# Optimization experiments

Measured on AMD Instinct MI355X. Metric: run time of the kernel, lower is better.

Reference implementation:

```python
import jax, jax.numpy as jnp
import numpy as np

N = 50000   # nodes
E = 600000  # edges
R = 8       # relations
B = 8       # bases
D = 128     # feature dim (in = hidden = out)
H = 4       # GAT heads
NEG = 0.1   # leaky_relu slope between layers
LN_EPS = 1e-5


def layer_norm(x, g, b):
    mu = jnp.mean(x, axis=-1, keepdims=True)
    var = jnp.mean(jnp.square(x - mu), axis=-1, keepdims=True)
    return (x - mu) * jax.lax.rsqrt(var + LN_EPS) * g + b


def rgcn(x, basis, comp, root, bias, src, dst, etype):
    # W[r] = sum_b comp[r,b] * basis[b]  -> [R, D, D]
    W = jnp.einsum('rb,bio->rio', comp, basis)
    h = jnp.einsum('ni,rio->rno', x, W)          # [R, N, D] per-relation transform
    msg = h[etype, src]                          # [E, D] gather per edge
    seg = etype.astype(jnp.int32) * N + dst      # (relation, dst) segment id
    deg = jax.ops.segment_sum(jnp.ones((src.shape[0],), x.dtype), seg, num_segments=R * N)
    inv = 1.0 / jnp.maximum(deg, 1.0)            # mean aggregation per relation
    out = jax.ops.segment_sum(msg * inv[seg][:, None], dst, num_segments=N)
    return out + x @ root + bias


def gat(x, W, a_src, a_dst, bias, src, dst):
    h = (x @ W).reshape(N, H, D)                 # [N, H, D]
    loop = jnp.arange(N, dtype=src.dtype)        # add self loops
    s2 = jnp.concatenate([src, loop])
    d2 = jnp.concatenate([dst, loop])
    hs = h[s2]                                   # [E+N, H, D]
    e = jnp.sum(hs * a_src, -1) + jnp.sum(h[d2] * a_dst, -1)   # [E+N, H]
    e = jax.nn.leaky_relu(e, 0.2)
    m = jax.ops.segment_max(e, d2, num_segments=N)              # stable softmax per dst
    ex = jnp.exp(e - m[d2])
    denom = jax.ops.segment_sum(ex, d2, num_segments=N)
    coef = ex / denom[d2]                        # [E+N, H]
    out = jax.ops.segment_sum(coef[..., None] * hs, d2, num_segments=N)  # [N, H, D]
    return jnp.mean(out, axis=1) + bias          # concat=False -> head mean


def setup_inputs():
    key = jax.random.key(0)
    ks = jax.random.split(key, 20)
    nrm = lambda k, shp, s=0.1: jax.random.normal(k, shp, dtype=jnp.float32) * s
    inp = {
        'x': jax.random.normal(ks[0], (N, D), dtype=jnp.float32),
        'edge_index': jax.random.randint(ks[1], (2, E), 0, N, dtype=jnp.int32),
        'edge_type': jax.random.randint(ks[2], (E,), 0, R, dtype=jnp.int32),
        'r0_basis': nrm(ks[3], (B, D, D)), 'r0_comp': nrm(ks[4], (R, B)),
        'r0_root': nrm(ks[5], (D, D)), 'r0_bias': jnp.zeros((D,), jnp.float32),
        'ln0_g': jnp.ones((D,), jnp.float32), 'ln0_b': jnp.zeros((D,), jnp.float32),
        'r1_basis': nrm(ks[6], (B, D, D)), 'r1_comp': nrm(ks[7], (R, B)),
        'r1_root': nrm(ks[8], (D, D)), 'r1_bias': jnp.zeros((D,), jnp.float32),
        'ln1_g': jnp.ones((D,), jnp.float32), 'ln1_b': jnp.zeros((D,), jnp.float32),
        'gat_w': nrm(ks[9], (D, H * D)), 'gat_asrc': nrm(ks[10], (H, D)),
        'gat_adst': nrm(ks[11], (H, D)), 'gat_bias': jnp.zeros((D,), jnp.float32),
        'ln2_g': jnp.ones((D,), jnp.float32), 'ln2_b': jnp.zeros((D,), jnp.float32),
        'r2_basis': nrm(ks[12], (B, D, D)), 'r2_comp': nrm(ks[13], (R, B)),
        'r2_root': nrm(ks[14], (D, D)), 'r2_bias': jnp.zeros((D,), jnp.float32),
    }
    return inp


def reference(x, edge_index, edge_type,
              r0_basis, r0_comp, r0_root, r0_bias, ln0_g, ln0_b,
              r1_basis, r1_comp, r1_root, r1_bias, ln1_g, ln1_b,
              gat_w, gat_asrc, gat_adst, gat_bias, ln2_g, ln2_b,
              r2_basis, r2_comp, r2_root, r2_bias):
    src, dst = edge_index[0], edge_index[1]
    h = rgcn(x, r0_basis, r0_comp, r0_root, r0_bias, src, dst, edge_type)
    h = jax.nn.leaky_relu(layer_norm(h, ln0_g, ln0_b), NEG)
    h = rgcn(h, r1_basis, r1_comp, r1_root, r1_bias, src, dst, edge_type)
    h = jax.nn.leaky_relu(layer_norm(h, ln1_g, ln1_b), NEG)
    h = gat(h, gat_w, gat_asrc, gat_adst, gat_bias, src, dst)
    h = jax.nn.leaky_relu(layer_norm(h, ln2_g, ln2_b), NEG)
    h = rgcn(h, r2_basis, r2_comp, r2_root, r2_bias, src, dst, edge_type)
    # F.normalize(p=2, dim=1)
    return h / jnp.maximum(jnp.linalg.norm(h, axis=1, keepdims=True), 1e-12)
```

## Files before the change

kernel.cpp:

```cpp
#include <hip/hip_runtime.h>
#include <hip/hip_bf16.h>

#define DD 128
#define NKEY8 8
#define LDA_AGG 1056
#define SRCM 0x00FFFFFF

using bf16x8 = __attribute__((ext_vector_type(8))) __bf16;
using f32x4  = __attribute__((ext_vector_type(4))) float;

__device__ __forceinline__ float leaky(float x, float s){ return x > 0.f ? x : s * x; }
__device__ __forceinline__ float bflo(unsigned u){ return __uint_as_float(u << 16); }
__device__ __forceinline__ float bfhi(unsigned u){ return __uint_as_float(u & 0xffff0000u); }
__device__ __forceinline__ unsigned bfpack(float x, float y){
  __hip_bfloat16 hx = __float2bfloat16(x), hy = __float2bfloat16(y);
  unsigned short ux = *reinterpret_cast<unsigned short*>(&hx);
  unsigned short uy = *reinterpret_cast<unsigned short*>(&hy);
  return (unsigned)ux | ((unsigned)uy << 16);
}

__global__ void k_hist(const int* __restrict__ dst, const int* __restrict__ et,
                       int* __restrict__ cnt, int E_){
  int e = blockIdx.x * 256 + threadIdx.x;
  if (e < E_) atomicAdd(&cnt[dst[e] * NKEY8 + et[e]], 1);
}

__global__ void k_scan1(const int* __restrict__ cnt, int* __restrict__ ptr,
                        int* __restrict__ part, int n){
  __shared__ int sm[256];
  int tid = threadIdx.x;
  int base = blockIdx.x * 1024 + tid * 4;
  int a0 = base + 0 < n ? cnt[base + 0] : 0;
  int a1 = base + 1 < n ? cnt[base + 1] : 0;
  int a2 = base + 2 < n ? cnt[base + 2] : 0;
  int a3 = base + 3 < n ? cnt[base + 3] : 0;
  int s = a0 + a1 + a2 + a3;
  sm[tid] = s; __syncthreads();
  for (int off = 1; off < 256; off <<= 1){
    int v = tid >= off ? sm[tid - off] : 0;
    __syncthreads(); sm[tid] += v; __syncthreads();
  }
  int ex = sm[tid] - s;
  if (tid == 255) part[blockIdx.x] = sm[255];
  if (base + 0 < n) ptr[base + 0] = ex;
  if (base + 1 < n) ptr[base + 1] = ex + a0;
  if (base + 2 < n) ptr[base + 2] = ex + a0 + a1;
  if (base + 3 < n) ptr[base + 3] = ex + a0 + a1 + a2;
}

__global__ void k_scan2(int* __restrict__ part, int nb){
  __shared__ int sm[512];
  int tid = threadIdx.x;
  int v = tid < nb ? part[tid] : 0;
  sm[tid] = v; __syncthreads();
  for (int off = 1; off < 512; off <<= 1){
    int u = tid >= off ? sm[tid - off] : 0;
    __syncthreads(); sm[tid] += u; __syncthreads();
  }
  if (tid < nb) part[tid] = sm[tid] - v;
}

__global__ void k_scan3(int* __restrict__ ptr, const int* __restrict__ part, int n, int E_){
  int i = blockIdx.x * 256 + threadIdx.x;
  if (i < n) ptr[i] += part[i >> 10];
  if (i == n) ptr[n] = E_;
}

__global__ void k_inv(const int* __restrict__ ptr, float* __restrict__ inv, int n){
  int i = blockIdx.x * 256 + threadIdx.x;
  if (i < n) inv[i] = 1.0f / fmaxf((float)(ptr[i + 1] - ptr[i]), 1.0f);
}

__global__ void k_scatter_pos(const int* __restrict__ src, const int* __restrict__ dst,
                              const int* __restrict__ et, int* __restrict__ run,
                              int* __restrict__ epk, int E_){
  int e = blockIdx.x * 256 + threadIdx.x;
  if (e >= E_) return;
  int r = et[e];
  int pos = atomicAdd(&run[dst[e] * NKEY8 + r], 1);
  epk[pos] = (r << 24) | src[e];
}

__global__ void k_cvt(const float* __restrict__ in, __hip_bfloat16* __restrict__ out, int n){
  int i = blockIdx.x * 256 + threadIdx.x;
  if (i < n) out[i] = __float2bfloat16(in[i]);
}

__global__ void k_makeW(const float* __restrict__ basis, const float* __restrict__ comp,
                        const float* __restrict__ root, __hip_bfloat16* __restrict__ Wp){
  int idx = blockIdx.x * 256 + threadIdx.x;
  int k = idx >> 7, n = idx & 127;
  float v;
  if (k < 1024){
    int r = k >> 7, i = k & 127;
    float s = 0.f;
    #pragma unroll
    for (int b = 0; b < 8; b++) s += comp[r * 8 + b] * basis[b * 16384 + i * 128 + n];
    v = s;
  } else {
    v = root[(k - 1024) * 128 + n];
  }
  int kt = k >> 5, kr = k & 31;
  int lane = (n & 15) | ((kr >> 3) << 4);
  int ii = kr & 7, nt = n >> 4;
  Wp[((size_t)(kt * 8 + nt) * 64 + lane) * 8 + ii] = __float2bfloat16(v);
}

__global__ void k_packGZ(const float* __restrict__ Wg, __hip_bfloat16* __restrict__ Wp){
  int idx = blockIdx.x * 256 + threadIdx.x;
  int k = idx >> 7, n = idx & 127;
  int h = k >> 7, i = k & 127;
  float v = Wg[(size_t)i * 512 + h * 128 + n];
  int kt = k >> 5, kr = k & 31;
  int lane = (n & 15) | ((kr >> 3) << 4);
  int ii = kr & 7, nt = n >> 4;
  Wp[((size_t)(kt * 8 + nt) * 64 + lane) * 8 + ii] = __float2bfloat16(v);
}

__global__ void k_valpha(const float* __restrict__ Wg, const float* __restrict__ a_src,
                         const float* __restrict__ a_dst, float* __restrict__ vT){
  int id = blockIdx.x * 256 + threadIdx.x;
  int sd = id >> 9, h = (id >> 7) & 3, i = id & 127;
  const float* a = (sd ? a_dst : a_src) + h * 128;
  const float* w = Wg + (size_t)i * 512 + h * 128;
  float s = 0.f;
  #pragma unroll 4
  for (int o = 0; o < 128; o++) s += w[o] * a[o];
  vT[(size_t)sd * 512 + h * 128 + i] = s;
}

__global__ void k_av(const __hip_bfloat16* __restrict__ xb, const float* __restrict__ vT,
                     float* __restrict__ aS, float* __restrict__ aD, int N_){
  int node = blockIdx.x * 4 + (threadIdx.x >> 6);
  if (node >= N_) return;
  int lane = threadIdx.x & 63;
  int h = lane >> 4, dg = lane & 15;
  uint4 u = *(const uint4*)(xb + (size_t)node * DD + dg * 8);
  const float* vs = vT + h * 128 + dg * 8;
  const float* vd = vT + 512 + h * 128 + dg * 8;
  float ss = 0.f, sd = 0.f;
  #pragma unroll
  for (int w = 0; w < 4; w++){
    unsigned uw = ((const unsigned*)&u)[w];
    float f0 = bflo(uw), f1 = bfhi(uw);
    ss += f0 * vs[w * 2] + f1 * vs[w * 2 + 1];
    sd += f0 * vd[w * 2] + f1 * vd[w * 2 + 1];
  }
  for (int o = 1; o < 16; o <<= 1){ ss += __shfl_xor(ss, o); sd += __shfl_xor(sd, o); }
  if (dg == 0){ aS[(size_t)node * 4 + h] = ss; aD[(size_t)node * 4 + h] = sd; }
}

__global__ void k_csr_agg(const int* __restrict__ ptr, const int* __restrict__ epk,
                          const float* __restrict__ inv, const __hip_bfloat16* __restrict__ xb,
                          __hip_bfloat16* __restrict__ agg, int N_){
  int w = threadIdx.x >> 6, lane = threadIdx.x & 63;
  int t = blockIdx.x * 4 + w;
  if (t >= N_) return;
  int beg = ptr[t * 8], end = ptr[t * 8 + 8];
  const __hip_bfloat16* xcol = xb + lane * 2;
  __hip_bfloat16* aggrow = agg + (size_t)t * LDA_AGG + lane * 2;
  const float* invrow = inv + (size_t)t * 8;
  float a0 = 0.f, a1 = 0.f;
  int cur = -1;
  unsigned written = 0;

#define CSR_FLUSH() { float iv = invrow[cur]; \
    *(unsigned*)(aggrow + cur * 128) = bfpack(a0 * iv, a1 * iv); \
    written |= (1u << cur); }
#define CSR_PROC(PK, U) { int r_ = (PK) >> 24; \
    if (r_ != cur){ if (cur >= 0){ CSR_FLUSH(); } cur = r_; a0 = 0.f; a1 = 0.f; } \
    a0 += bflo(U); a1 += bfhi(U); }

  int e = beg;
  for (; e + 4 <= end; e += 4){
    int pk0 = epk[e], pk1 = epk[e + 1], pk2 = epk[e + 2], pk3 = epk[e + 3];
    unsigned u0 = *(const unsigned*)(xcol + (size_t)(pk0 & SRCM) * DD);
    unsigned u1 = *(const unsigned*)(xcol + (size_t)(pk1 & SRCM) * DD);
    unsigned u2 = *(const unsigned*)(xcol + (size_t)(pk2 & SRCM) * DD);
    unsigned u3 = *(const unsigned*)(xcol + (size_t)(pk3 & SRCM) * DD);
    CSR_PROC(pk0, u0); CSR_PROC(pk1, u1); CSR_PROC(pk2, u2); CSR_PROC(pk3, u3);
  }
  for (; e < end; e++){
    int pk0 = epk[e];
    unsigned u0 = *(const unsigned*)(xcol + (size_t)(pk0 & SRCM) * DD);
    CSR_PROC(pk0, u0);
  }
  if (cur >= 0){ CSR_FLUSH(); }
  #pragma unroll
  for (int r = 0; r < 8; r++)
    if (!(written & (1u << r))) *(unsigned*)(aggrow + r * 128) = 0u;
#undef CSR_PROC
#undef CSR_FLUSH
}

__global__ void k_zagg(const int* __restrict__ ptr, const int* __restrict__ epk,
                       const float* __restrict__ cf, const float* __restrict__ cfS,
                       const float* __restrict__ den, const __hip_bfloat16* __restrict__ xb,
                       __hip_bfloat16* __restrict__ z, int N_){
  int w = threadIdx.x >> 6, lane = threadIdx.x & 63;
  int t = blockIdx.x * 4 + w;
  if (t >= N_) return;
  int dg = lane & 31, ep = lane >> 5;
  int beg = ptr[t * 8], end = ptr[t * 8 + 8];
  float acc[4][4];
  #pragma unroll
  for (int h = 0; h < 4; h++)
    #pragma unroll
    for (int j = 0; j < 4; j++) acc[h][j] = 0.f;
  const __hip_bfloat16* xbase = xb + dg * 4;
  for (int e = beg + ep; e < end; e += 2){
    int s = epk[e] & SRCM;
    uint2 v = *(const uint2*)(xbase + (size_t)s * DD);
    float4 c = *(const float4*)(cf + (size_t)e * 4);
    float f0 = bflo(v.x), f1 = bfhi(v.x), f2 = bflo(v.y), f3 = bfhi(v.y);
    const float* cp = (const float*)&c;
    #pragma unroll
    for (int h = 0; h < 4; h++){
      acc[h][0] += cp[h] * f0; acc[h][1] += cp[h] * f1;
      acc[h][2] += cp[h] * f2; acc[h][3] += cp[h] * f3;
    }
  }
  #pragma unroll
  for (int h = 0; h < 4; h++)
    #pragma unroll
    for (int j = 0; j < 4; j++) acc[h][j] += __shfl_xor(acc[h][j], 32);
  if (ep == 0){
    uint2 v = *(const uint2*)(xbase + (size_t)t * DD);
    float f0 = bflo(v.x), f1 = bfhi(v.x), f2 = bflo(v.y), f3 = bfhi(v.y);
    float4 cs = *(const float4*)(cfS + (size_t)t * 4);
    float4 dn = *(const float4*)(den + (size_t)t * 4);
    const float* csp = (const float*)&cs;
    const float* dnp = (const float*)&dn;
    #pragma unroll
    for (int h = 0; h < 4; h++){
      float sc = 0.25f / dnp[h];
      float y0 = (acc[h][0] + csp[h] * f0) * sc;
      float y1 = (acc[h][1] + csp[h] * f1) * sc;
      float y2 = (acc[h][2] + csp[h] * f2) * sc;
      float y3 = (acc[h][3] + csp[h] * f3) * sc;
      uint2 o; o.x = bfpack(y0, y1); o.y = bfpack(y2, y3);
      *(uint2*)(z + (size_t)t * 512 + h * 128 + dg * 4) = o;
    }
  }
}

template<int MODE>
__launch_bounds__(256)
__global__ void k_gemm_mfma(const __hip_bfloat16* __restrict__ A1, int lda1, int K1,
                            const __hip_bfloat16* __restrict__ A2, int K2,
                            int M, const __hip_bfloat16* __restrict__ Bp, int ntt,
                            const float* __restrict__ bias,
                            const float* __restrict__ ln_g, const float* __restrict__ ln_b,
                            float* __restrict__ Cf, __hip_bfloat16* __restrict__ Cb,
                            int ldc){
  int wave = threadIdx.x >> 6, lane = threadIdx.x & 63;
  int nt0 = blockIdx.y << 3;
  int mbase = blockIdx.x * 128 + wave * 32;
  int r0 = min(mbase + (lane & 15), M - 1);
  int r1 = min(mbase + 16 + (lane & 15), M - 1);
  int koff = (lane >> 4) << 3;
  f32x4 acc[2][8];
  #pragma unroll
  for (int i = 0; i < 2; i++)
    #pragma unroll
    for (int j = 0; j < 8; j++) acc[i][j] = (f32x4){0.f, 0.f, 0.f, 0.f};

  int ktile = 0;
  {
    const __hip_bfloat16* a0p = A1 + (size_t)r0 * lda1 + koff;
    const __hip_bfloat16* a1p = A1 + (size_t)r1 * lda1 + koff;
    for (int k0 = 0; k0 < K1; k0 += 32, ++ktile){
      bf16x8 a0 = *(const bf16x8*)(a0p + k0);
      bf16x8 a1 = *(const bf16x8*)(a1p + k0);
      const bf16x8* bfr = (const bf16x8*)(Bp + (((size_t)ktile * ntt + nt0) * 64 + lane) * 8);
      #pragma unroll
      for (int nt = 0; nt < 8; nt++){
        bf16x8 b = bfr[(size_t)nt * 64];
        acc[0][nt] = __builtin_amdgcn_mfma_f32_16x16x32_bf16(a0, b, acc[0][nt], 0, 0, 0);
        acc[1][nt] = __builtin_amdgcn_mfma_f32_16x16x32_bf16(a1, b, acc[1][nt], 0, 0, 0);
      }
    }
  }
  if (A2){
    const __hip_bfloat16* a0p = A2 + (size_t)r0 * DD + koff;
    const __hip_bfloat16* a1p = A2 + (size_t)r1 * DD + koff;
    for (int k0 = 0; k0 < K2; k0 += 32, ++ktile){
      bf16x8 a0 = *(const bf16x8*)(a0p + k0);
      bf16x8 a1 = *(const bf16x8*)(a1p + k0);
      const bf16x8* bfr = (const bf16x8*)(Bp + (((size_t)ktile * ntt + nt0) * 64 + lane) * 8);
      #pragma unroll
      for (int nt = 0; nt < 8; nt++){
        bf16x8 b = bfr[(size_t)nt * 64];
        acc[0][nt] = __builtin_amdgcn_mfma_f32_16x16x32_bf16(a0, b, acc[0][nt], 0, 0, 0);
        acc[1][nt] = __builtin_amdgcn_mfma_f32_16x16x32_bf16(a1, b, acc[1][nt], 0, 0, 0);
      }
    }
  }

  const int colb = lane & 15;
  const int lq = lane >> 4;

  float bias8[8], g8[8], b8[8];
  #pragma unroll
  for (int nt = 0; nt < 8; nt++){
    int c = (nt << 4) + colb;
    bias8[nt] = bias ? bias[c] : 0.f;
    if (MODE == 1){ g8[nt] = ln_g[c]; b8[nt] = ln_b[c]; }
  }

  #pragma unroll
  for (int mt = 0; mt < 2; mt++){
    #pragma unroll
    for (int j = 0; j < 4; j++){
      int row = mbase + mt * 16 + lq * 4 + j;
      if (MODE == 1){
        float v[8]; float s = 0.f;
        #pragma unroll
        for (int nt = 0; nt < 8; nt++){ v[nt] = acc[mt][nt][j] + bias8[nt]; s += v[nt]; }
        #pragma unroll
        for (int o = 1; o < 16; o <<= 1) s += __shfl_xor(s, o);
        float mu = s * (1.f / 128.f);
        float q = 0.f;
        #pragma unroll
        for (int nt = 0; nt < 8; nt++){ float dd = v[nt] - mu; q += dd * dd; }
        #pragma unroll
        for (int o = 1; o < 16; o <<= 1) q += __shfl_xor(q, o);
        float rstd = rsqrtf(q * (1.f / 128.f) + 1e-5f);
        if (row < M){
          #pragma unroll
          for (int nt = 0; nt < 8; nt++){
            float y = leaky((v[nt] - mu) * rstd * g8[nt] + b8[nt], 0.1f);
            Cb[(size_t)row * ldc + (nt << 4) + colb] = __float2bfloat16(y);
          }
        }
      } else {
        float v[8]; float q = 0.f;
        #pragma unroll
        for (int nt = 0; nt < 8; nt++){ v[nt] = acc[mt][nt][j] + bias8[nt]; q += v[nt] * v[nt]; }
        #pragma unroll
        for (int o = 1; o < 16; o <<= 1) q += __shfl_xor(q, o);
        float sc = 1.0f / fmaxf(sqrtf(q), 1e-12f);
        if (row < M){
          #pragma unroll
          for (int nt = 0; nt < 8; nt++)
            Cf[(size_t)row * ldc + (nt << 4) + colb] = v[nt] * sc;
        }
      }
    }
  }
}

__global__ void k_gat_coef(const int* __restrict__ ptr, const int* __restrict__ epk,
                           const float* __restrict__ aS, const float* __restrict__ aD,
                           float* __restrict__ cf, float* __restrict__ cfS,
                           float* __restrict__ den, int N_){
  int id = blockIdx.x * 256 + threadIdx.x;
  int t = id >> 2, h = id & 3;
  if (t >= N_) return;
  int beg = ptr[t * 8], end = ptr[t * 8 + 8];
  float adh = aD[(size_t)t * 4 + h];
  float ash = aS[(size_t)t * 4 + h];
  float selfe = leaky(ash + adh, 0.2f);
  float m = selfe;
  for (int e = beg; e < end; e++){
    int s = epk[e] & SRCM;
    m = fmaxf(m, leaky(aS[(size_t)s * 4 + h] + adh, 0.2f));
  }
  float sv = __expf(selfe - m);
  cfS[(size_t)t * 4 + h] = sv;
  float d = sv;
  for (int e = beg; e < end; e++){
    int s = epk[e] & SRCM;
    float x = __expf(leaky(aS[(size_t)s * 4 + h] + adh, 0.2f) - m);
    cf[(size_t)e * 4 + h] = x;
    d += x;
  }
  den[(size_t)t * 4 + h] = d;
}

extern "C" void kernel_launch(void* const* d_in, const int* in_sizes, int n_in,
                              void* d_out, int out_size, void* d_ws, size_t ws_size,
                              hipStream_t stream){
  const float* x       = (const float*)d_in[0];
  const int*   ei      = (const int*)d_in[1];
  const int*   et      = (const int*)d_in[2];
  const float* r0_basis= (const float*)d_in[3];  const float* r0_comp = (const float*)d_in[4];
  const float* r0_root = (const float*)d_in[5];  const float* r0_bias = (const float*)d_in[6];
  const float* ln0_g   = (const float*)d_in[7];  const float* ln0_b   = (const float*)d_in[8];
  const float* r1_basis= (const float*)d_in[9];  const float* r1_comp = (const float*)d_in[10];
  const float* r1_root = (const float*)d_in[11]; const float* r1_bias = (const float*)d_in[12];
  const float* ln1_g   = (const float*)d_in[13]; const float* ln1_b   = (const float*)d_in[14];
  const float* gat_w   = (const float*)d_in[15]; const float* gat_asrc= (const float*)d_in[16];
  const float* gat_adst= (const float*)d_in[17]; const float* gat_bias= (const float*)d_in[18];
  const float* ln2_g   = (const float*)d_in[19]; const float* ln2_b   = (const float*)d_in[20];
  const float* r2_basis= (const float*)d_in[21]; const float* r2_comp = (const float*)d_in[22];
  const float* r2_root = (const float*)d_in[23]; const float* r2_bias = (const float*)d_in[24];

  const int N_ = in_sizes[0] / DD;
  const int E_ = in_sizes[2];
  const int NK = N_ * NKEY8;
  const int* src = ei;
  const int* dst = ei + E_;
  float* T2 = (float*)d_out;

  char* wp_ = (char*)d_ws;
  auto alloc = [&](size_t b)->void*{ void* p = wp_; wp_ += (b + 255) & ~(size_t)255; return p; };
  __hip_bfloat16* agg16 = (__hip_bfloat16*)alloc((size_t)N_ * LDA_AGG * 2);
  __hip_bfloat16* xb16  = (__hip_bfloat16*)alloc((size_t)N_ * DD * 2);
  float*          inv   = (float*)alloc((size_t)NK * 4);
  int*            ptrb  = (int*)alloc((size_t)(NK + 1) * 4);
  int*            cnt   = (int*)alloc((size_t)NK * 4);
  int*            run   = (int*)alloc((size_t)NK * 4);
  int*            epk   = (int*)alloc((size_t)E_ * 4);
  int*            part  = (int*)alloc(512 * 4);
  float*          aS    = (float*)alloc((size_t)N_ * 4 * 4);
  float*          aD    = (float*)alloc((size_t)N_ * 4 * 4);
  float*          cf    = (float*)alloc((size_t)E_ * 4 * 4);
  float*          cfS   = (float*)alloc((size_t)N_ * 4 * 4);
  float*          den   = (float*)alloc((size_t)N_ * 4 * 4);
  float*          vT    = (float*)alloc((size_t)2 * 512 * 4);
  __hip_bfloat16* Wp    = (__hip_bfloat16*)alloc((size_t)1152 * 128 * 2);
  __hip_bfloat16* WpZ   = (__hip_bfloat16*)alloc((size_t)512 * 128 * 2);
  if ((size_t)(wp_ - (char*)d_ws) > ws_size) return;
  __hip_bfloat16* z16 = agg16;

  const int Mb = (N_ + 127) / 128;
  const int nScanB = (NK + 1023) / 1024;

  hipMemsetAsync(cnt, 0, (size_t)NK * 4, stream);
  k_hist<<<(E_ + 255) / 256, 256, 0, stream>>>(dst, et, cnt, E_);
  k_scan1<<<nScanB, 256, 0, stream>>>(cnt, ptrb, part, NK);
  k_scan2<<<1, 512, 0, stream>>>(part, nScanB);
  k_scan3<<<(NK + 1 + 255) / 256, 256, 0, stream>>>(ptrb, part, NK, E_);
  k_inv<<<(NK + 255) / 256, 256, 0, stream>>>(ptrb, inv, NK);
  hipMemcpyAsync(run, ptrb, (size_t)NK * 4, hipMemcpyDeviceToDevice, stream);
  k_scatter_pos<<<(E_ + 255) / 256, 256, 0, stream>>>(src, dst, et, run, epk, E_);
  k_cvt<<<(N_ * DD + 255) / 256, 256, 0, stream>>>(x, xb16, N_ * DD);

  k_makeW<<<576, 256, 0, stream>>>(r0_basis, r0_comp, r0_root, Wp);
  k_csr_agg<<<(N_ + 3) / 4, 256, 0, stream>>>(ptrb, epk, inv, xb16, agg16, N_);
  k_gemm_mfma<1><<<dim3(Mb, 1), 256, 0, stream>>>(agg16, LDA_AGG, 1024, xb16, 128, N_, Wp, 8,
      r0_bias, ln0_g, ln0_b, nullptr, xb16, DD);

  k_makeW<<<576, 256, 0, stream>>>(r1_basis, r1_comp, r1_root, Wp);
  k_csr_agg<<<(N_ + 3) / 4, 256, 0, stream>>>(ptrb, epk, inv, xb16, agg16, N_);
  k_gemm_mfma<1><<<dim3(Mb, 1), 256, 0, stream>>>(agg16, LDA_AGG, 1024, xb16, 128, N_, Wp, 8,
      r1_bias, ln1_g, ln1_b, nullptr, xb16, DD);

  k_valpha<<<4, 256, 0, stream>>>(gat_w, gat_asrc, gat_adst, vT);
  k_packGZ<<<256, 256, 0, stream>>>(gat_w, WpZ);
  k_av<<<(N_ + 3) / 4, 256, 0, stream>>>(xb16, vT, aS, aD, N_);
  k_gat_coef<<<(N_ * 4 + 255) / 256, 256, 0, stream>>>(ptrb, epk, aS, aD, cf, cfS, den, N_);
  k_zagg<<<(N_ + 3) / 4, 256, 0, stream>>>(ptrb, epk, cf, cfS, den, xb16, z16, N_);
  k_gemm_mfma<1><<<dim3(Mb, 1), 256, 0, stream>>>(z16, 512, 512, nullptr, 0, N_, WpZ, 8,
      gat_bias, ln2_g, ln2_b, nullptr, xb16, DD);

  k_makeW<<<576, 256, 0, stream>>>(r2_basis, r2_comp, r2_root, Wp);
  k_csr_agg<<<(N_ + 3) / 4, 256, 0, stream>>>(ptrb, epk, inv, xb16, agg16, N_);
  k_gemm_mfma<3><<<dim3(Mb, 1), 256, 0, stream>>>(agg16, LDA_AGG, 1024, xb16, 128, N_, Wp, 8,
      r2_bias, nullptr, nullptr, T2, nullptr, DD);
}
```

Baseline: 464.0 us.

## Fuse RGCN CSR aggregation into MFMA GEMM via shared-memory staging

Replaces the separate per-relation CSR aggregation kernel and the GEMM for each RGCN layer with one fused kernel. The fused kernel aggregates 64 nodes' per-relation means, two relations at a time, into an LDS tile and feeds it straight into MFMA, then adds the root term and the LayerNorm or L2-normalise epilogue. This avoids writing and re-reading the large N×1056 bf16 aggregation buffer each layer. In exchange it needs ping-pong feature buffers, and the gather phase and the MFMA phase inside a block are serialised by barriers, which can lower occupancy and overlap.

After: 578.1 us. 24.6% more time.

```diff
diff --git a/kernel.cpp b/kernel.cpp
--- a/kernel.cpp
+++ b/kernel.cpp
@@ -3,7 +3,6 @@
 
 #define DD 128
 #define NKEY8 8
-#define LDA_AGG 1056
 #define SRCM 0x00FFFFFF
 
 using bf16x8 = __attribute__((ext_vector_type(8))) __bf16;
@@ -150,47 +149,134 @@
   if (dg == 0){ aS[(size_t)node * 4 + h] = ss; aD[(size_t)node * 4 + h] = sd; }
 }
 
-__global__ void k_csr_agg(const int* __restrict__ ptr, const int* __restrict__ epk,
-                          const float* __restrict__ inv, const __hip_bfloat16* __restrict__ xb,
-                          __hip_bfloat16* __restrict__ agg, int N_){
-  int w = threadIdx.x >> 6, lane = threadIdx.x & 63;
-  int t = blockIdx.x * 4 + w;
-  if (t >= N_) return;
-  int beg = ptr[t * 8], end = ptr[t * 8 + 8];
-  const __hip_bfloat16* xcol = xb + lane * 2;
-  __hip_bfloat16* aggrow = agg + (size_t)t * LDA_AGG + lane * 2;
-  const float* invrow = inv + (size_t)t * 8;
-  float a0 = 0.f, a1 = 0.f;
-  int cur = -1;
-  unsigned written = 0;
-
-#define CSR_FLUSH() { float iv = invrow[cur]; \
-    *(unsigned*)(aggrow + cur * 128) = bfpack(a0 * iv, a1 * iv); \
-    written |= (1u << cur); }
-#define CSR_PROC(PK, U) { int r_ = (PK) >> 24; \
-    if (r_ != cur){ if (cur >= 0){ CSR_FLUSH(); } cur = r_; a0 = 0.f; a1 = 0.f; } \
-    a0 += bflo(U); a1 += bfhi(U); }
-
-  int e = beg;
-  for (; e + 4 <= end; e += 4){
-    int pk0 = epk[e], pk1 = epk[e + 1], pk2 = epk[e + 2], pk3 = epk[e + 3];
-    unsigned u0 = *(const unsigned*)(xcol + (size_t)(pk0 & SRCM) * DD);
-    unsigned u1 = *(const unsigned*)(xcol + (size_t)(pk1 & SRCM) * DD);
-    unsigned u2 = *(const unsigned*)(xcol + (size_t)(pk2 & SRCM) * DD);
-    unsigned u3 = *(const unsigned*)(xcol + (size_t)(pk3 & SRCM) * DD);
-    CSR_PROC(pk0, u0); CSR_PROC(pk1, u1); CSR_PROC(pk2, u2); CSR_PROC(pk3, u3);
-  }
-  for (; e < end; e++){
-    int pk0 = epk[e];
-    unsigned u0 = *(const unsigned*)(xcol + (size_t)(pk0 & SRCM) * DD);
-    CSR_PROC(pk0, u0);
-  }
-  if (cur >= 0){ CSR_FLUSH(); }
-  #pragma unroll
-  for (int r = 0; r < 8; r++)
-    if (!(written & (1u << r))) *(unsigned*)(aggrow + r * 128) = 0u;
-#undef CSR_PROC
-#undef CSR_FLUSH
+template<int MODE>
+__launch_bounds__(256)
+__global__ void k_rgcn_fused(const int* __restrict__ ptr, const int* __restrict__ epk,
+                             const float* __restrict__ inv, const __hip_bfloat16* __restrict__ xin,
+                             const __hip_bfloat16* __restrict__ Bp,
+                             const float* __restrict__ bias,
+                             const float* __restrict__ ln_g, const float* __restrict__ ln_b,
+                             float* __restrict__ Cf, __hip_bfloat16* __restrict__ Cb,
+                             int N_){
+  __shared__ __hip_bfloat16 As[64][264];
+  const int wave = threadIdx.x >> 6, lane = threadIdx.x & 63;
+  const int m0 = blockIdx.x * 64;
+  const int hw = lane >> 5, sl = lane & 31;
+  const int mrow = wave * 16 + (lane & 15);
+  const int lq = lane >> 4;
+  const __hip_bfloat16* xcol4 = xin + sl * 4;
+
+  f32x4 acc[8];
+  #pragma unroll
+  for (int nt = 0; nt < 8; nt++) acc[nt] = (f32x4){0.f, 0.f, 0.f, 0.f};
+
+  for (int p = 0; p < 4; p++){
+    __syncthreads();
+    for (int i = 0; i < 8; i++){
+      int trow = wave * 16 + i * 2 + hw;
+      int t = m0 + trow;
+      unsigned wm = 0;
+      float a0 = 0.f, a1 = 0.f, a2 = 0.f, a3 = 0.f;
+      int cur = -1;
+      if (t < N_){
+        int beg = ptr[t * 8 + 2 * p], end = ptr[t * 8 + 2 * p + 2];
+
+#define FLUSH2() { float iv = inv[t * 8 + cur]; int rl_ = cur - 2 * p; \
+    uint2 o_; o_.x = bfpack(a0 * iv, a1 * iv); o_.y = bfpack(a2 * iv, a3 * iv); \
+    *(uint2*)&As[trow][rl_ * 128 + sl * 4] = o_; wm |= 1u << rl_; }
+#define PROC2(PK, U) { int r_ = (PK) >> 24; \
+    if (r_ != cur){ if (cur >= 0){ FLUSH2(); } cur = r_; a0 = a1 = a2 = a3 = 0.f; } \
+    a0 += bflo((U).x); a1 += bfhi((U).x); a2 += bflo((U).y); a3 += bfhi((U).y); }
+
+        int e = beg;
+        for (; e + 2 <= end; e += 2){
+          int pk0 = epk[e], pk1 = epk[e + 1];
+          uint2 u0 = *(const uint2*)(xcol4 + (size_t)(pk0 & SRCM) * DD);
+          uint2 u1 = *(const uint2*)(xcol4 + (size_t)(pk1 & SRCM) * DD);
+          PROC2(pk0, u0); PROC2(pk1, u1);
+        }
+        if (e < end){
+          int pk0 = epk[e];
+          uint2 u0 = *(const uint2*)(xcol4 + (size_t)(pk0 & SRCM) * DD);
+          PROC2(pk0, u0);
+        }
+        if (cur >= 0){ FLUSH2(); }
+#undef PROC2
+#undef FLUSH2
+      }
+      uint2 z_; z_.x = 0u; z_.y = 0u;
+      if (!(wm & 1u)) *(uint2*)&As[trow][0 * 128 + sl * 4] = z_;
+      if (!(wm & 2u)) *(uint2*)&As[trow][1 * 128 + sl * 4] = z_;
+    }
+    __syncthreads();
+    #pragma unroll
+    for (int kt = 0; kt < 8; kt++){
+      bf16x8 a = *(const bf16x8*)&As[mrow][kt * 32 + lq * 8];
+      const bf16x8* bfr = (const bf16x8*)(Bp + (((size_t)(p * 8 + kt) * 8) * 64 + lane) * 8);
+      #pragma unroll
+      for (int nt = 0; nt < 8; nt++)
+        acc[nt] = __builtin_amdgcn_mfma_f32_16x16x32_bf16(a, bfr[(size_t)nt * 64], acc[nt], 0, 0, 0);
+    }
+  }
+
+  {
+    int r0 = min(m0 + mrow, N_ - 1);
+    const __hip_bfloat16* ap = xin + (size_t)r0 * DD + lq * 8;
+    #pragma unroll
+    for (int kt = 0; kt < 4; kt++){
+      bf16x8 a = *(const bf16x8*)(ap + kt * 32);
+      const bf16x8* bfr = (const bf16x8*)(Bp + (((size_t)(32 + kt) * 8) * 64 + lane) * 8);
+      #pragma unroll
+      for (int nt = 0; nt < 8; nt++)
+        acc[nt] = __builtin_amdgcn_mfma_f32_16x16x32_bf16(a, bfr[(size_t)nt * 64], acc[nt], 0, 0, 0);
+    }
+  }
+
+  const int colb = lane & 15;
+  float bias8[8], g8[8], b8[8];
+  #pragma unroll
+  for (int nt = 0; nt < 8; nt++){
+    int c = (nt << 4) + colb;
+    bias8[nt] = bias ? bias[c] : 0.f;
+    if (MODE == 1){ g8[nt] = ln_g[c]; b8[nt] = ln_b[c]; }
+  }
+  #pragma unroll
+  for (int j = 0; j < 4; j++){
+    int row = m0 + wave * 16 + lq * 4 + j;
+    if (MODE == 1){
+      float v[8]; float s = 0.f;
+      #pragma unroll
+      for (int nt = 0; nt < 8; nt++){ v[nt] = acc[nt][j] + bias8[nt]; s += v[nt]; }
+      #pragma unroll
+      for (int o = 1; o < 16; o <<= 1) s += __shfl_xor(s, o);
+      float mu = s * (1.f / 128.f);
+      float q = 0.f;
+      #pragma unroll
+      for (int nt = 0; nt < 8; nt++){ float dd = v[nt] - mu; q += dd * dd; }
+      #pragma unroll
+      for (int o = 1; o < 16; o <<= 1) q += __shfl_xor(q, o);
+      float rstd = rsqrtf(q * (1.f / 128.f) + 1e-5f);
+      if (row < N_){
+        #pragma unroll
+        for (int nt = 0; nt < 8; nt++){
+          float y = leaky((v[nt] - mu) * rstd * g8[nt] + b8[nt], 0.1f);
+          Cb[(size_t)row * DD + (nt << 4) + colb] = __float2bfloat16(y);
+        }
+      }
+    } else {
+      float v[8]; float q = 0.f;
+      #pragma unroll
+      for (int nt = 0; nt < 8; nt++){ v[nt] = acc[nt][j] + bias8[nt]; q += v[nt] * v[nt]; }
+      #pragma unroll
+      for (int o = 1; o < 16; o <<= 1) q += __shfl_xor(q, o);
+      float sc = 1.0f / fmaxf(sqrtf(q), 1e-12f);
+      if (row < N_){
+        #pragma unroll
+        for (int nt = 0; nt < 8; nt++)
+          Cf[(size_t)row * DD + (nt << 4) + colb] = v[nt] * sc;
+      }
+    }
+  }
 }
 
 __global__ void k_zagg(const int* __restrict__ ptr, const int* __restrict__ epk,
@@ -244,15 +330,12 @@
   }
 }
 
-template<int MODE>
 __launch_bounds__(256)
 __global__ void k_gemm_mfma(const __hip_bfloat16* __restrict__ A1, int lda1, int K1,
-                            const __hip_bfloat16* __restrict__ A2, int K2,
                             int M, const __hip_bfloat16* __restrict__ Bp, int ntt,
                             const float* __restrict__ bias,
                             const float* __restrict__ ln_g, const float* __restrict__ ln_b,
-                            float* __restrict__ Cf, __hip_bfloat16* __restrict__ Cb,
-                            int ldc){
+                            __hip_bfloat16* __restrict__ Cb, int ldc){
   int wave = threadIdx.x >> 6, lane = threadIdx.x & 63;
   int nt0 = blockIdx.y << 3;
   int mbase = blockIdx.x * 128 + wave * 32;
@@ -266,84 +349,51 @@
     for (int j = 0; j < 8; j++) acc[i][j] = (f32x4){0.f, 0.f, 0.f, 0.f};
 
   int ktile = 0;
-  {
-    const __hip_bfloat16* a0p = A1 + (size_t)r0 * lda1 + koff;
-    const __hip_bfloat16* a1p = A1 + (size_t)r1 * lda1 + koff;
-    for (int k0 = 0; k0 < K1; k0 += 32, ++ktile){
-      bf16x8 a0 = *(const bf16x8*)(a0p + k0);
-      bf16x8 a1 = *(const bf16x8*)(a1p + k0);
-      const bf16x8* bfr = (const bf16x8*)(Bp + (((size_t)ktile * ntt + nt0) * 64 + lane) * 8);
-      #pragma unroll
-      for (int nt = 0; nt < 8; nt++){
-        bf16x8 b = bfr[(size_t)nt * 64];
-        acc[0][nt] = __builtin_amdgcn_mfma_f32_16x16x32_bf16(a0, b, acc[0][nt], 0, 0, 0);
-        acc[1][nt] = __builtin_amdgcn_mfma_f32_16x16x32_bf16(a1, b, acc[1][nt], 0, 0, 0);
-      }
-    }
-  }
-  if (A2){
-    const __hip_bfloat16* a0p = A2 + (size_t)r0 * DD + koff;
-    const __hip_bfloat16* a1p = A2 + (size_t)r1 * DD + koff;
-    for (int k0 = 0; k0 < K2; k0 += 32, ++ktile){
-      bf16x8 a0 = *(const bf16x8*)(a0p + k0);
-      bf16x8 a1 = *(const bf16x8*)(a1p + k0);
-      const bf16x8* bfr = (const bf16x8*)(Bp + (((size_t)ktile * ntt + nt0) * 64 + lane) * 8);
-      #pragma unroll
-      for (int nt = 0; nt < 8; nt++){
-        bf16x8 b = bfr[(size_t)nt * 64];
-        acc[0][nt] = __builtin_amdgcn_mfma_f32_16x16x32_bf16(a0, b, acc[0][nt], 0, 0, 0);
-        acc[1][nt] = __builtin_amdgcn_mfma_f32_16x16x32_bf16(a1, b, acc[1][nt], 0, 0, 0);
-      }
+  const __hip_bfloat16* a0p = A1 + (size_t)r0 * lda1 + koff;
+  const __hip_bfloat16* a1p = A1 + (size_t)r1 * lda1 + koff;
+  for (int k0 = 0; k0 < K1; k0 += 32, ++ktile){
+    bf16x8 a0 = *(const bf16x8*)(a0p + k0);
+    bf16x8 a1 = *(const bf16x8*)(a1p + k0);
+    const bf16x8* bfr = (const bf16x8*)(Bp + (((size_t)ktile * ntt + nt0) * 64 + lane) * 8);
+    #pragma unroll
+    for (int nt = 0; nt < 8; nt++){
+      bf16x8 b = bfr[(size_t)nt * 64];
+      acc[0][nt] = __builtin_amdgcn_mfma_f32_16x16x32_bf16(a0, b, acc[0][nt], 0, 0, 0);
+      acc[1][nt] = __builtin_amdgcn_mfma_f32_16x16x32_bf16(a1, b, acc[1][nt], 0, 0, 0);
     }
   }
 
   const int colb = lane & 15;
   const int lq = lane >> 4;
-
   float bias8[8], g8[8], b8[8];
   #pragma unroll
   for (int nt = 0; nt < 8; nt++){
     int c = (nt << 4) + colb;
     bias8[nt] = bias ? bias[c] : 0.f;
-    if (MODE == 1){ g8[nt] = ln_g[c]; b8[nt] = ln_b[c]; }
-  }
-
+    g8[nt] = ln_g[c]; b8[nt] = ln_b[c];
+  }
   #pragma unroll
   for (int mt = 0; mt < 2; mt++){
     #pragma unroll
     for (int j = 0; j < 4; j++){
       int row = mbase + mt * 16 + lq * 4 + j;
-      if (MODE == 1){
-        float v[8]; float s = 0.f;
+      float v[8]; float s = 0.f;
+      #pragma unroll
+      for (int nt = 0; nt < 8; nt++){ v[nt] = acc[mt][nt][j] + bias8[nt]; s += v[nt]; }
+      #pragma unroll
+      for (int o = 1; o < 16; o <<= 1) s += __shfl_xor(s, o);
+      float mu = s * (1.f / 128.f);
+      float q = 0.f;
+      #pragma unroll
+      for (int nt = 0; nt < 8; nt++){ float dd = v[nt] - mu; q += dd * dd; }
+      #pragma unroll
+      for (int o = 1; o < 16; o <<= 1) q += __shfl_xor(q, o);
+      float rstd = rsqrtf(q * (1.f / 128.f) + 1e-5f);
+      if (row < M){
         #pragma unroll
-        for (int nt = 0; nt < 8; nt++){ v[nt] = acc[mt][nt][j] + bias8[nt]; s += v[nt]; }
-        #pragma unroll
-        for (int o = 1; o < 16; o <<= 1) s += __shfl_xor(s, o);
-        float mu = s * (1.f / 128.f);
-        float q = 0.f;
-        #pragma unroll
-        for (int nt = 0; nt < 8; nt++){ float dd = v[nt] - mu; q += dd * dd; }
-        #pragma unroll
-        for (int o = 1; o < 16; o <<= 1) q += __shfl_xor(q, o);
-        float rstd = rsqrtf(q * (1.f / 128.f) + 1e-5f);
-        if (row < M){
-          #pragma unroll
-          for (int nt = 0; nt < 8; nt++){
-            float y = leaky((v[nt] - mu) * rstd * g8[nt] + b8[nt], 0.1f);
-            Cb[(size_t)row * ldc + (nt << 4) + colb] = __float2bfloat16(y);
-          }
-        }
-      } else {
-        float v[8]; float q = 0.f;
-        #pragma unroll
-        for (int nt = 0; nt < 8; nt++){ v[nt] = acc[mt][nt][j] + bias8[nt]; q += v[nt] * v[nt]; }
-        #pragma unroll
-        for (int o = 1; o < 16; o <<= 1) q += __shfl_xor(q, o);
-        float sc = 1.0f / fmaxf(sqrtf(q), 1e-12f);
-        if (row < M){
-          #pragma unroll
-          for (int nt = 0; nt < 8; nt++)
-            Cf[(size_t)row * ldc + (nt << 4) + colb] = v[nt] * sc;
+        for (int nt = 0; nt < 8; nt++){
+          float y = leaky((v[nt] - mu) * rstd * g8[nt] + b8[nt], 0.1f);
+          Cb[(size_t)row * ldc + (nt << 4) + colb] = __float2bfloat16(y);
         }
       }
     }
@@ -405,8 +455,9 @@
 
   char* wp_ = (char*)d_ws;
   auto alloc = [&](size_t b)->void*{ void* p = wp_; wp_ += (b + 255) & ~(size_t)255; return p; };
-  __hip_bfloat16* agg16 = (__hip_bfloat16*)alloc((size_t)N_ * LDA_AGG * 2);
-  __hip_bfloat16* xb16  = (__hip_bfloat16*)alloc((size_t)N_ * DD * 2);
+  __hip_bfloat16* z16   = (__hip_bfloat16*)alloc((size_t)N_ * 512 * 2);
+  __hip_bfloat16* xb0   = (__hip_bfloat16*)alloc((size_t)N_ * DD * 2);
+  __hip_bfloat16* xb1   = (__hip_bfloat16*)alloc((size_t)N_ * DD * 2);
   float*          inv   = (float*)alloc((size_t)NK * 4);
   int*            ptrb  = (int*)alloc((size_t)(NK + 1) * 4);
   int*            cnt   = (int*)alloc((size_t)NK * 4);
@@ -422,9 +473,9 @@
   __hip_bfloat16* Wp    = (__hip_bfloat16*)alloc((size_t)1152 * 128 * 2);
   __hip_bfloat16* WpZ   = (__hip_bfloat16*)alloc((size_t)512 * 128 * 2);
   if ((size_t)(wp_ - (char*)d_ws) > ws_size) return;
-  __hip_bfloat16* z16 = agg16;
-
-  const int Mb = (N_ + 127) / 128;
+
+  const int MbF = (N_ + 63) / 64;
+  const int Mb  = (N_ + 127) / 128;
   const int nScanB = (NK + 1023) / 1024;
 
   hipMemsetAsync(cnt, 0, (size_t)NK * 4, stream);
@@ -435,28 +486,24 @@
   k_inv<<<(NK + 255) / 256, 256, 0, stream>>>(ptrb, inv, NK);
   hipMemcpyAsync(run, ptrb, (size_t)NK * 4, hipMemcpyDeviceToDevice, stream);
   k_scatter_pos<<<(E_ + 255) / 256, 256, 0, stream>>>(src, dst, et, run, epk, E_);
-  k_cvt<<<(N_ * DD + 255) / 256, 256, 0, stream>>>(x, xb16, N_ * DD);
+  k_cvt<<<(N_ * DD + 255) / 256, 256, 0, stream>>>(x, xb0, N_ * DD);
 
   k_makeW<<<576, 256, 0, stream>>>(r0_basis, r0_comp, r0_root, Wp);
-  k_csr_agg<<<(N_ + 3) / 4, 256, 0, stream>>>(ptrb, epk, inv, xb16, agg16, N_);
-  k_gemm_mfma<1><<<dim3(Mb, 1), 256, 0, stream>>>(agg16, LDA_AGG, 1024, xb16, 128, N_, Wp, 8,
-      r0_bias, ln0_g, ln0_b, nullptr, xb16, DD);
-
+  k_rgcn_fused<1><<<MbF, 256, 0, stream>>>(ptrb, epk, inv, xb0, Wp, r0_bias,
+                                           ln0_g, ln0_b, nullptr, xb1, N_);
   k_makeW<<<576, 256, 0, stream>>>(r1_basis, r1_comp, r1_root, Wp);
-  k_csr_agg<<<(N_ + 3) / 4, 256, 0, stream>>>(ptrb, epk, inv, xb16, agg16, N_);
-  k_gemm_mfma<1><<<dim3(Mb, 1), 256, 0, stream>>>(agg16, LDA_AGG, 1024, xb16, 128, N_, Wp, 8,
-      r1_bias, ln1_g, ln1_b, nullptr, xb16, DD);
+  k_rgcn_fused<1><<<MbF, 256, 0, stream>>>(ptrb, epk, inv, xb1, Wp, r1_bias,
+                                           ln1_g, ln1_b, nullptr, xb0, N_);
 
   k_valpha<<<4, 256, 0, stream>>>(gat_w, gat_asrc, gat_adst, vT);
   k_packGZ<<<256, 256, 0, stream>>>(gat_w, WpZ);
-  k_av<<<(N_ + 3) / 4, 256, 0, stream>>>(xb16, vT, aS, aD, N_);
+  k_av<<<(N_ + 3) / 4, 256, 0, stream>>>(xb0, vT, aS, aD, N_);
   k_gat_coef<<<(N_ * 4 + 255) / 256, 256, 0, stream>>>(ptrb, epk, aS, aD, cf, cfS, den, N_);
-  k_zagg<<<(N_ + 3) / 4, 256, 0, stream>>>(ptrb, epk, cf, cfS, den, xb16, z16, N_);
-  k_gemm_mfma<1><<<dim3(Mb, 1), 256, 0, stream>>>(z16, 512, 512, nullptr, 0, N_, WpZ, 8,
-      gat_bias, ln2_g, ln2_b, nullptr, xb16, DD);
+  k_zagg<<<(N_ + 3) / 4, 256, 0, stream>>>(ptrb, epk, cf, cfS, den, xb0, z16, N_);
+  k_gemm_mfma<<<dim3(Mb, 1), 256, 0, stream>>>(z16, 512, 512, N_, WpZ, 8,
+      gat_bias, ln2_g, ln2_b, xb1, DD);
 
   k_makeW<<<576, 256, 0, stream>>>(r2_basis, r2_comp, r2_root, Wp);
-  k_csr_agg<<<(N_ + 3) / 4, 256, 0, stream>>>(ptrb, epk, inv, xb16, agg16, N_);
-  k_gemm_mfma<3><<<dim3(Mb, 1), 256, 0, stream>>>(agg16, LDA_AGG, 1024, xb16, 128, N_, Wp, 8,
-      r2_bias, nullptr, nullptr, T2, nullptr, DD);
-}
+  k_rgcn_fused<3><<<MbF, 256, 0, stream>>>(ptrb, epk, inv, xb1, Wp, r2_bias,
+                                           nullptr, nullptr, T2, nullptr, N_);
+}
```
